# Performance work log

Hardware: AMD Instinct MI355X
Metric: run time of the kernel (lower is better)

Reference implementation:

```python
import jax, jax.numpy as jnp
import numpy as np

B, S, D, H = 4, 2048, 1024, 16
DH = D // H


def _rope_tables():
    # standard RoPE angle tables, shaped [1, S, 1, DH] as the module expects
    inv_freq = 1.0 / (10000.0 ** (np.arange(0, DH, 2, dtype=np.float32) / DH))
    ang = np.arange(S, dtype=np.float32)[:, None] * inv_freq[None, :]  # [S, DH/2]
    ang = np.concatenate([ang, ang], axis=-1)  # [S, DH]
    cos = jnp.asarray(np.cos(ang))[None, :, None, :]
    sin = jnp.asarray(np.sin(ang))[None, :, None, :]
    return cos, sin


def setup_inputs() -> dict:
    key = jax.random.key(0)
    ks = jax.random.split(key, 5)
    x = jax.random.normal(ks[0], (B, S, D), dtype=jnp.float32)
    wq = jax.random.normal(ks[1], (D, D), dtype=jnp.float32) * 0.02
    wk = jax.random.normal(ks[2], (D, D), dtype=jnp.float32) * 0.02
    wv = jax.random.normal(ks[3], (D, D), dtype=jnp.float32) * 0.02
    wo = jax.random.normal(ks[4], (D, D), dtype=jnp.float32) * 0.02
    cos, sin = _rope_tables()
    return {"x": x, "cos": cos, "sin": sin, "wq": wq, "wk": wk, "wv": wv, "wo": wo}


def _rotate_half(t):
    t1, t2 = t[..., : DH // 2], t[..., DH // 2:]
    return jnp.concatenate([-t2, t1], axis=-1)


def reference(x, cos, sin, wq, wk, wv, wo):
    b, s, d = x.shape
    # QKV projections (torch Linear: y = x @ W.T), reshape to [B, H, S, DH]
    q = (x @ wq.T).reshape(b, s, H, DH).transpose(0, 2, 1, 3)
    k = (x @ wk.T).reshape(b, s, H, DH).transpose(0, 2, 1, 3)
    v = (x @ wv.T).reshape(b, s, H, DH).transpose(0, 2, 1, 3)
    # permute(0,2,1,3): [1,S,1,DH] -> [1,1,S,DH]; slice [:, :s] is a no-op on the size-1 head dim
    cos_p = jnp.transpose(cos, (0, 2, 1, 3))[:, :s]
    sin_p = jnp.transpose(sin, (0, 2, 1, 3))[:, :s]
    q = q * cos_p + _rotate_half(q) * sin_p
    k = k * cos_p + _rotate_half(k) * sin_p
    # SDPA (no mask, dropout_p = 0)
    scores = jnp.einsum("bhqd,bhkd->bhqk", q, k) / jnp.sqrt(jnp.float32(DH))
    attn = jax.nn.softmax(scores, axis=-1)
    out = jnp.einsum("bhqk,bhkd->bhqd", attn, v)
    out = out.transpose(0, 2, 1, 3).reshape(b, s, d)
    return out @ wo.T
```

## Files before the change

kernel.cpp:

```cpp
#include <hip/hip_runtime.h>
#include <hip/hip_bf16.h>
#include <stdint.h>

#define B 4
#define S 2048
#define D 1024
#define H 16
#define DH 64
#define M_TOT (B*S)
#define BH (B*H)

typedef unsigned short u16;
typedef unsigned int u32;
typedef __attribute__((ext_vector_type(4))) float f32x4;
typedef __attribute__((ext_vector_type(16))) float f32x16;
typedef __attribute__((ext_vector_type(8))) short bf16x8;
typedef __attribute__((ext_vector_type(2))) unsigned int u32x2;

typedef const __attribute__((address_space(1))) unsigned int* gp_t;
typedef __attribute__((address_space(3))) unsigned int* lp_t;

__device__ __forceinline__ void gload_lds16(const void* g, void* l) {
    __builtin_amdgcn_global_load_lds((gp_t)g, (lp_t)l, 16, 0, 0);
}

__device__ __forceinline__ float bf2f(u16 u) {
    u32 t = ((u32)u) << 16;
    float f; __builtin_memcpy(&f, &t, 4); return f;
}
__device__ __forceinline__ u16 f2bf(float f) {
    u32 u; __builtin_memcpy(&u, &f, 4);
    u += 0x7fffu + ((u >> 16) & 1u);
    return (u16)(u >> 16);
}
__device__ __forceinline__ u32 packbf(float lo, float hi_) {
    __hip_bfloat162 h = __float22bfloat162_rn(float2{lo, hi_});
    u32 r; __builtin_memcpy(&r, &h, 4); return r;
}

__device__ __forceinline__ float exp2_fast(float x) { return __builtin_amdgcn_exp2f(x); }

#if __has_builtin(__builtin_amdgcn_permlane32_swap)
__device__ __forceinline__ void plswap(u32& a, u32& bb) {
    u32x2 r = __builtin_amdgcn_permlane32_swap(a, bb, false, false);
    a = r.x; bb = r.y;
}
#else
__device__ __forceinline__ void plswap(u32& a, u32& bb) {
    int hi = (threadIdx.x >> 5) & 1;
    u32 ra = (u32)__shfl_xor((int)a, 32);
    u32 rb = (u32)__shfl_xor((int)bb, 32);
    u32 na = hi ? rb : a;
    u32 nb = hi ? bb : ra;
    a = na; bb = nb;
}
#endif

__global__ __launch_bounds__(256)
void cvt_all_kernel(const float* __restrict__ x,
                    const float* __restrict__ wq, const float* __restrict__ wk,
                    const float* __restrict__ wv, const float* __restrict__ wo,
                    u16* __restrict__ xb, u16* __restrict__ wqb, u16* __restrict__ wkb,
                    u16* __restrict__ wvb, u16* __restrict__ wob)
{
    const size_t MD = (size_t)M_TOT * D;
    const size_t WD = (size_t)D * D;
    size_t i = ((size_t)blockIdx.x * 256 + threadIdx.x) * 8;
    const float* src; u16* dst; size_t off;
    if (i < MD) { src = x; dst = xb; off = i; }
    else {
        size_t j = i - MD;
        int wsel = (int)(j >> 20);
        off = j & (WD - 1);
        if      (wsel == 0) { src = wq; dst = wqb; }
        else if (wsel == 1) { src = wk; dst = wkb; }
        else if (wsel == 2) { src = wv; dst = wvb; }
        else                { src = wo; dst = wob; }
    }
    float4 a = *(const float4*)(src + off);
    float4 b = *(const float4*)(src + off + 4);
    union { u16 u[8]; bf16x8 v; } o;
    o.u[0] = f2bf(a.x); o.u[1] = f2bf(a.y); o.u[2] = f2bf(a.z); o.u[3] = f2bf(a.w);
    o.u[4] = f2bf(b.x); o.u[5] = f2bf(b.y); o.u[6] = f2bf(b.z); o.u[7] = f2bf(b.w);
    *(bf16x8*)(dst + off) = o.v;
}

template<int WRITE_BF16, int DO_ROPE>
__global__ __launch_bounds__(256)
void gemm_mfma(const u16* __restrict__ X,
               const u16* __restrict__ W0, const u16* __restrict__ W1, const u16* __restrict__ W2,
               void* Y0, void* Y1, void* Y2,
               const float* __restrict__ cosT, const float* __restrict__ sinT)
{
    __shared__ __align__(16) u16 Al[128 * 32];
    __shared__ __align__(16) u16 Bl[128 * 32];

    const u16* Wm = (blockIdx.z == 0) ? W0 : (blockIdx.z == 1) ? W1 : W2;
    void* Yv      = (blockIdx.z == 0) ? Y0 : (blockIdx.z == 1) ? Y1 : Y2;

    const int t = threadIdx.x;
    const int w = t >> 6, ll = t & 63;
    const int wr = w >> 1, wc = w & 1;
    const int g = ll >> 4, lc = ll & 15;
    const int m0 = blockIdx.x * 128, n0 = blockIdx.y * 128;

    const int srow = t >> 2;
    const int scol = (t & 3) * 8;

    const u16* Xa = X + (size_t)m0 * D;
    const u16* Wa = Wm + (size_t)n0 * D;

    f32x4 acc[4][4];
    #pragma unroll
    for (int i = 0; i < 4; ++i)
        #pragma unroll
        for (int j = 0; j < 4; ++j)
            acc[i][j] = (f32x4){0.f, 0.f, 0.f, 0.f};

    for (int k0 = 0; k0 < D; k0 += 32) {
        gload_lds16(Xa + (size_t)(srow)      * D + k0 + scol, &Al[(w * 64) * 8]);
        gload_lds16(Xa + (size_t)(64 + srow) * D + k0 + scol, &Al[(256 + w * 64) * 8]);
        gload_lds16(Wa + (size_t)(srow)      * D + k0 + scol, &Bl[(w * 64) * 8]);
        gload_lds16(Wa + (size_t)(64 + srow) * D + k0 + scol, &Bl[(256 + w * 64) * 8]);
        __syncthreads();

        bf16x8 af[4], bf[4];
        #pragma unroll
        for (int i = 0; i < 4; ++i)
            af[i] = *(const bf16x8*)&Al[(wr * 64 + i * 16 + lc) * 32 + g * 8];
        #pragma unroll
        for (int j = 0; j < 4; ++j)
            bf[j] = *(const bf16x8*)&Bl[(wc * 64 + j * 16 + lc) * 32 + g * 8];

        #pragma unroll
        for (int i = 0; i < 4; ++i)
            #pragma unroll
            for (int j = 0; j < 4; ++j)
                acc[i][j] = __builtin_amdgcn_mfma_f32_16x16x32_bf16(af[i], bf[j], acc[i][j], 0, 0, 0);
        __syncthreads();
    }

    if (DO_ROPE) {
        const float scale = (blockIdx.z == 0) ? (0.125f * 1.44269504f) : 1.0f;
        u16* Y = (u16*)Yv;
        #pragma unroll
        for (int i = 0; i < 4; ++i)
            #pragma unroll
            for (int r = 0; r < 4; ++r) {
                int row = m0 + wr * 64 + i * 16 + g * 4 + r;
                int s = row & (S - 1);
                #pragma unroll
                for (int jh = 0; jh < 2; ++jh) {
                    float c  = cosT[s * DH + jh * 16 + lc];
                    float sn = sinT[s * DH + jh * 16 + lc];
                    float a0 = acc[i][jh][r], a1 = acc[i][jh + 2][r];
                    size_t base = (size_t)row * D + n0 + wc * 64;
                    Y[base + jh * 16 + lc]       = f2bf((a0 * c - a1 * sn) * scale);
                    Y[base + (jh + 2) * 16 + lc] = f2bf((a1 * c + a0 * sn) * scale);
                }
            }
    } else if (WRITE_BF16) {
        u16* Y = (u16*)Yv;
        #pragma unroll
        for (int i = 0; i < 4; ++i)
            #pragma unroll
            for (int j = 0; j < 4; ++j)
                #pragma unroll
                for (int r = 0; r < 4; ++r) {
                    int row = m0 + wr * 64 + i * 16 + g * 4 + r;
                    int col = n0 + wc * 64 + j * 16 + lc;
                    Y[(size_t)row * D + col] = f2bf(acc[i][j][r]);
                }
    } else {
        float* Y = (float*)Yv;
        #pragma unroll
        for (int i = 0; i < 4; ++i)
            #pragma unroll
            for (int j = 0; j < 4; ++j)
                #pragma unroll
                for (int r = 0; r < 4; ++r) {
                    int row = m0 + wr * 64 + i * 16 + g * 4 + r;
                    int col = n0 + wc * 64 + j * 16 + lc;
                    Y[(size_t)row * D + col] = acc[i][j][r];
                }
    }
}

__global__ __launch_bounds__(256)
void vtrans_kernel(const u16* __restrict__ V, u16* __restrict__ Vt)
{
    __shared__ __align__(16) u16 Tl[64][72];
    const int t = threadIdx.x;
    const int s0 = blockIdx.x * 64;
    const int bh = blockIdx.y;
    const int b = bh >> 4, h = bh & 15;

    int sl = t >> 2, dh0 = (t & 3) * 16;
    const u16* src = &V[(size_t)(b * S + s0 + sl) * D + h * DH + dh0];
    bf16x8 v0 = *(const bf16x8*)src;
    bf16x8 v1 = *(const bf16x8*)(src + 8);
    #pragma unroll
    for (int i = 0; i < 8; ++i) {
        Tl[sl][dh0 + i]     = ((u16*)&v0)[i];
        Tl[sl][dh0 + 8 + i] = ((u16*)&v1)[i];
    }
    __syncthreads();
    int dh = t >> 2, ss0 = (t & 3) * 16;
    union { u16 u[16]; } o;
    #pragma unroll
    for (int i = 0; i < 16; ++i) o.u[i] = Tl[ss0 + i][dh];
    u16* dst = &Vt[((size_t)bh * DH + dh) * S + s0 + ss0];
    *(bf16x8*)dst       = *(bf16x8*)&o.u[0];
    *(bf16x8*)(dst + 8) = *(bf16x8*)&o.u[8];
}

#define QBLK 256
#define NT (S / 64)

__global__ __launch_bounds__(256, 2)
void attn_mfma(const u16* __restrict__ Q, const u16* __restrict__ Kg,
               const u16* __restrict__ Vt, u16* __restrict__ CTX)
{
    __shared__ __align__(16) u16 smem[16384];

    const int t  = threadIdx.x;
    const int w  = t >> 6;
    const int q  = t & 31;
    const int hi = (t >> 5) & 1;

    const int bid  = blockIdx.x;
    const int xcd  = bid & 7;
    const int slot = bid >> 3;
    const int bh   = xcd * 8 + (slot >> 3);
    const int qb   = slot & 7;
    const int b = bh >> 4, h = bh & 15;
    const int q0 = qb * QBLK;
    const int qbase = q0 + w * 64;

    bf16x8 qf[2][4];
    #pragma unroll
    for (int qg = 0; qg < 2; ++qg) {
        const u16* qp = &Q[(size_t)(b*S + qbase + qg*32 + q) * D + h*DH + hi*8];
        qf[qg][0] = *(const bf16x8*)(qp);
        qf[qg][1] = *(const bf16x8*)(qp + 16);
        qf[qg][2] = *(const bf16x8*)(qp + 32);
        qf[qg][3] = *(const bf16x8*)(qp + 48);
    }

    bf16x8 ones;
    {
        union { u16 u[8]; bf16x8 v; } ou;
        #pragma unroll
        for (int i = 0; i < 8; ++i) ou.u[i] = 0x3f80;
        ones = ou.v;
    }

    f32x16 po[4], lsum[2];
    #pragma unroll
    for (int i = 0; i < 16; ++i) {
        po[0][i] = 0.f; po[1][i] = 0.f; po[2][i] = 0.f; po[3][i] = 0.f;
        lsum[0][i] = 0.f; lsum[1][i] = 0.f;
    }

    const int srow = t >> 3;
    const int kbs  = ((t & 7) << 4) ^ ((srow & 7) << 4);
    const int scol = kbs >> 1;
    const int rsw  = (q & 7) << 4;

    u16* buf0 = smem;
    u16* buf1 = smem + 8192;

    const u16* kg = Kg + ((size_t)(b * S) + srow) * D + (size_t)h * DH + scol;
    const u16* vg = Vt + ((size_t)bh * DH + srow) * S + scol;
    const size_t KADV = (size_t)64 * D;

    #define STAGE(dst) do {                                   \
        gload_lds16(kg,           (dst) + w*512);             \
        gload_lds16(kg + 32*D,    (dst) + 2048 + w*512);      \
        gload_lds16(vg,           (dst) + 4096 + w*512);      \
        gload_lds16(vg + 32*S,    (dst) + 4096 + 2048 + w*512); \
        kg += KADV; vg += 64; } while (0)

    auto compute = [&](const u16* base) {
        const u16* Kl = base;
        const u16* Vl = base + 4096;
        f32x16 p00, p01, p10, p11;
        #pragma unroll
        for (int i = 0; i < 16; ++i) { p00[i]=0.f; p01[i]=0.f; p10[i]=0.f; p11[i]=0.f; }
        __builtin_amdgcn_s_setprio(1);
        #pragma unroll
        for (int c = 0; c < 4; ++c) {
            int cb = ((c*32 + hi*16) ^ rsw) >> 1;
            bf16x8 k0 = *(const bf16x8*)&Kl[(q << 6) + cb];
            bf16x8 k1 = *(const bf16x8*)&Kl[((32 + q) << 6) + cb];
            p00 = __builtin_amdgcn_mfma_f32_32x32x16_bf16(k0, qf[0][c], p00, 0, 0, 0);
            p01 = __builtin_amdgcn_mfma_f32_32x32x16_bf16(k1, qf[0][c], p01, 0, 0, 0);
            p10 = __builtin_amdgcn_mfma_f32_32x32x16_bf16(k0, qf[1][c], p10, 0, 0, 0);
            p11 = __builtin_amdgcn_mfma_f32_32x32x16_bf16(k1, qf[1][c], p11, 0, 0, 0);
        }
        __builtin_amdgcn_s_setprio(0);

        bf16x8 pa[2][4];
        #pragma unroll
        for (int qg = 0; qg < 2; ++qg) {
            const f32x16& e0 = qg ? p10 : p00;
            const f32x16& e1 = qg ? p11 : p01;
            u32 WW[16];
            #pragma unroll
            for (int j = 0; j < 8; ++j) {
                WW[j]     = packbf(exp2_fast(e0[2*j]), exp2_fast(e0[2*j + 1]));
                WW[8 + j] = packbf(exp2_fast(e1[2*j]), exp2_fast(e1[2*j + 1]));
            }
            #pragma unroll
            for (int ks = 0; ks < 4; ++ks) {
                const int b4 = 4*(ks & 1) + 8*(ks >> 1);
                u32 w0 = WW[b4 + 0], w1 = WW[b4 + 1], w2 = WW[b4 + 2], w3 = WW[b4 + 3];
                plswap(w0, w2);
                plswap(w1, w3);
                union { u32 u[4]; bf16x8 v; } pb;
                pb.u[0] = w0; pb.u[1] = w1; pb.u[2] = w2; pb.u[3] = w3;
                pa[qg][ks] = pb.v;
            }
        }

        __builtin_amdgcn_s_setprio(1);
        #pragma unroll
        for (int ks = 0; ks < 4; ++ks) {
            lsum[0] = __builtin_amdgcn_mfma_f32_32x32x16_bf16(ones, pa[0][ks], lsum[0], 0, 0, 0);
            lsum[1] = __builtin_amdgcn_mfma_f32_32x32x16_bf16(ones, pa[1][ks], lsum[1], 0, 0, 0);
        }
        #pragma unroll
        for (int ks = 0; ks < 4; ++ks) {
            int vb = ((ks*32 + hi*16) ^ rsw) >> 1;
            bf16x8 v0 = *(const bf16x8*)&Vl[(q << 6) + vb];
            bf16x8 v1 = *(const bf16x8*)&Vl[((32 + q) << 6) + vb];
            po[0] = __builtin_amdgcn_mfma_f32_32x32x16_bf16(v0, pa[0][ks], po[0], 0, 0, 0);
            po[1] = __builtin_amdgcn_mfma_f32_32x32x16_bf16(v1, pa[0][ks], po[1], 0, 0, 0);
            po[2] = __builtin_amdgcn_mfma_f32_32x32x16_bf16(v0, pa[1][ks], po[2], 0, 0, 0);
            po[3] = __builtin_amdgcn_mfma_f32_32x32x16_bf16(v1, pa[1][ks], po[3], 0, 0, 0);
        }
        __builtin_amdgcn_s_setprio(0);
    };

    STAGE(buf0);
    asm volatile("s_waitcnt vmcnt(0)" ::: "memory");
    __builtin_amdgcn_s_barrier();

    for (int ti = 0; ti < NT; ti += 2) {
        STAGE(buf1);
        compute(buf0);
        asm volatile("s_waitcnt vmcnt(0)" ::: "memory");
        __builtin_amdgcn_s_barrier();
        if (ti < NT - 2) STAGE(buf0);
        compute(buf1);
        asm volatile("s_waitcnt vmcnt(0)" ::: "memory");
        __builtin_amdgcn_s_barrier();
    }
    #undef STAGE

    u16* ow = &smem[w * 2304];
    #pragma unroll
    for (int qg = 0; qg < 2; ++qg) {
        float inv = 1.f / lsum[qg][0];
        #pragma unroll
        for (int r = 0; r < 16; ++r) {
            int d0 = (r & 3) + 8 * (r >> 2) + 4 * hi;
            ow[q * 72 + d0]      = f2bf(po[qg*2 + 0][r] * inv);
            ow[q * 72 + 32 + d0] = f2bf(po[qg*2 + 1][r] * inv);
        }
        int row = (t & 63) >> 1, half = t & 1;
        const u16* orow = &ow[row * 72 + half * 32];
        u16* gp = &CTX[(size_t)(b*S + qbase + qg*32 + row) * D + h*DH + half * 32];
        #pragma unroll
        for (int i = 0; i < 4; ++i)
            *(bf16x8*)(gp + i * 8) = *(const bf16x8*)(orow + i * 8);
    }
}

extern "C" void kernel_launch(void* const* d_in, const int* in_sizes, int n_in,
                              void* d_out, int out_size, void* d_ws, size_t ws_size,
                              hipStream_t stream)
{
    const float* x    = (const float*)d_in[0];
    const float* cosT = (const float*)d_in[1];
    const float* sinT = (const float*)d_in[2];
    const float* wq   = (const float*)d_in[3];
    const float* wk   = (const float*)d_in[4];
    const float* wv   = (const float*)d_in[5];
    const float* wo   = (const float*)d_in[6];
    float* out = (float*)d_out;

    const size_t MD = (size_t)M_TOT * D;
    const size_t WD = (size_t)D * D;

    u16* xb   = (u16*)d_ws;
    u16* Qb   = xb + MD;
    u16* Kb   = Qb + MD;
    u16* Vb   = Kb + MD;
    u16* Vtb  = Vb + MD;
    u16* CTXb = Vtb + MD;
    u16* wqb  = CTXb + MD;
    u16* wkb  = wqb + WD;
    u16* wvb  = wkb + WD;
    u16* wob  = wvb + WD;

    cvt_all_kernel<<<(int)((MD + 4*WD) / 8 / 256), 256, 0, stream>>>(
        x, wq, wk, wv, wo, xb, wqb, wkb, wvb, wob);

    gemm_mfma<1, 1><<<dim3(M_TOT / 128, D / 128, 2), 256, 0, stream>>>(
        xb, wqb, wkb, nullptr, Qb, Kb, nullptr, cosT, sinT);
    gemm_mfma<1, 0><<<dim3(M_TOT / 128, D / 128, 1), 256, 0, stream>>>(
        xb, wvb, nullptr, nullptr, Vb, nullptr, nullptr, nullptr, nullptr);

    vtrans_kernel<<<dim3(S / 64, BH), 256, 0, stream>>>(Vb, Vtb);

    attn_mfma<<<dim3(M_TOT / QBLK * H), 256, 0, stream>>>(Qb, Kb, Vtb, CTXb);

    gemm_mfma<0, 0><<<dim3(M_TOT / 128, D / 128, 1), 256, 0, stream>>>(
        CTXb, wob, nullptr, nullptr, out, nullptr, nullptr, nullptr, nullptr);
}
```

Baseline: 204.4 us.

## Merge V projection into QK GEMM launch and split attention compute into halves

The V projection now runs in the same GEMM launch as Q and K by adding a third grid z-slice, and RoPE is skipped when z is 2, which removes one kernel launch and tail. Inside the attention kernel the per-tile QK^T is computed in two key halves. Exp/pack and PV MFMAs for the first half are issued before the second half's packing, so VALU work can interleave with MFMA work. Accumulators now start from a zero vector instead of being zeroed each tile, and row-sum MFMAs are folded into the PV loops. The price is more register pressure and more reliance on the compiler to schedule the interleaving.

```diff
diff --git a/kernel.cpp b/kernel.cpp
--- a/kernel.cpp
+++ b/kernel.cpp
@@ -140,7 +140,7 @@
         __syncthreads();
     }
 
-    if (DO_ROPE) {
+    if (DO_ROPE && blockIdx.z < 2) {
         const float scale = (blockIdx.z == 0) ? (0.125f * 1.44269504f) : 1.0f;
         u16* Y = (u16*)Yv;
         #pragma unroll
@@ -255,11 +255,11 @@
         ones = ou.v;
     }
 
-    f32x16 po[4], lsum[2];
+    f32x16 po[4], lsum[2], zv;
     #pragma unroll
     for (int i = 0; i < 16; ++i) {
         po[0][i] = 0.f; po[1][i] = 0.f; po[2][i] = 0.f; po[3][i] = 0.f;
-        lsum[0][i] = 0.f; lsum[1][i] = 0.f;
+        lsum[0][i] = 0.f; lsum[1][i] = 0.f; zv[i] = 0.f;
     }
 
     const int srow = t >> 3;
@@ -281,63 +281,97 @@
         gload_lds16(vg + 32*S,    (dst) + 4096 + 2048 + w*512); \
         kg += KADV; vg += 64; } while (0)
 
+    #define PACK_HALF(pqg0, pqg1, pa00, pa01, pa10, pa11) do {            \
+        u32 W0[8], W1[8];                                                  \
+        _Pragma("unroll")                                                  \
+        for (int j = 0; j < 8; ++j) {                                      \
+            W0[j] = packbf(exp2_fast((pqg0)[2*j]), exp2_fast((pqg0)[2*j+1]));\
+            W1[j] = packbf(exp2_fast((pqg1)[2*j]), exp2_fast((pqg1)[2*j+1]));\
+        }                                                                  \
+        plswap(W0[0], W0[2]); plswap(W0[1], W0[3]);                        \
+        plswap(W0[4], W0[6]); plswap(W0[5], W0[7]);                        \
+        plswap(W1[0], W1[2]); plswap(W1[1], W1[3]);                        \
+        plswap(W1[4], W1[6]); plswap(W1[5], W1[7]);                        \
+        { union { u32 u[4]; bf16x8 v; } pb;                                \
+          pb.u[0]=W0[0]; pb.u[1]=W0[1]; pb.u[2]=W0[2]; pb.u[3]=W0[3]; (pa00)=pb.v; \
+          pb.u[0]=W0[4]; pb.u[1]=W0[5]; pb.u[2]=W0[6]; pb.u[3]=W0[7]; (pa01)=pb.v; \
+          pb.u[0]=W1[0]; pb.u[1]=W1[1]; pb.u[2]=W1[2]; pb.u[3]=W1[3]; (pa10)=pb.v; \
+          pb.u[0]=W1[4]; pb.u[1]=W1[5]; pb.u[2]=W1[6]; pb.u[3]=W1[7]; (pa11)=pb.v; } \
+    } while (0)
+
     auto compute = [&](const u16* base) {
         const u16* Kl = base;
         const u16* Vl = base + 4096;
-        f32x16 p00, p01, p10, p11;
-        #pragma unroll
-        for (int i = 0; i < 16; ++i) { p00[i]=0.f; p01[i]=0.f; p10[i]=0.f; p11[i]=0.f; }
+
+        f32x16 p00, p10, p01, p11;
+        {
+            bf16x8 k0[4];
+            #pragma unroll
+            for (int c = 0; c < 4; ++c)
+                k0[c] = *(const bf16x8*)&Kl[(q << 6) + ((( c*32 + hi*16) ^ rsw) >> 1)];
+            __builtin_amdgcn_s_setprio(1);
+            p00 = __builtin_amdgcn_mfma_f32_32x32x16_bf16(k0[0], qf[0][0], zv, 0, 0, 0);
+            p10 = __builtin_amdgcn_mfma_f32_32x32x16_bf16(k0[0], qf[1][0], zv, 0, 0, 0);
+            #pragma unroll
+            for (int c = 1; c < 4; ++c) {
+                p00 = __builtin_amdgcn_mfma_f32_32x32x16_bf16(k0[c], qf[0][c], p00, 0, 0, 0);
+                p10 = __builtin_amdgcn_mfma_f32_32x32x16_bf16(k0[c], qf[1][c], p10, 0, 0, 0);
+            }
+            __builtin_amdgcn_s_setprio(0);
+        }
+        {
+            bf16x8 k1[4];
+            #pragma unroll
+            for (int c = 0; c < 4; ++c)
+                k1[c] = *(const bf16x8*)&Kl[((32 + q) << 6) + (((c*32 + hi*16) ^ rsw) >> 1)];
+            __builtin_amdgcn_s_setprio(1);
+            p01 = __builtin_amdgcn_mfma_f32_32x32x16_bf16(k1[0], qf[0][0], zv, 0, 0, 0);
+            p11 = __builtin_amdgcn_mfma_f32_32x32x16_bf16(k1[0], qf[1][0], zv, 0, 0, 0);
+            #pragma unroll
+            for (int c = 1; c < 4; ++c) {
+                p01 = __builtin_amdgcn_mfma_f32_32x32x16_bf16(k1[c], qf[0][c], p01, 0, 0, 0);
+                p11 = __builtin_amdgcn_mfma_f32_32x32x16_bf16(k1[c], qf[1][c], p11, 0, 0, 0);
+            }
+            __builtin_amdgcn_s_setprio(0);
+        }
+
+        bf16x8 pa00, pa01, pa10, pa11;
+        PACK_HALF(p00, p10, pa00, pa01, pa10, pa11);
+
         __builtin_amdgcn_s_setprio(1);
         #pragma unroll
-        for (int c = 0; c < 4; ++c) {
-            int cb = ((c*32 + hi*16) ^ rsw) >> 1;
-            bf16x8 k0 = *(const bf16x8*)&Kl[(q << 6) + cb];
-            bf16x8 k1 = *(const bf16x8*)&Kl[((32 + q) << 6) + cb];
-            p00 = __builtin_amdgcn_mfma_f32_32x32x16_bf16(k0, qf[0][c], p00, 0, 0, 0);
-            p01 = __builtin_amdgcn_mfma_f32_32x32x16_bf16(k1, qf[0][c], p01, 0, 0, 0);
-            p10 = __builtin_amdgcn_mfma_f32_32x32x16_bf16(k0, qf[1][c], p10, 0, 0, 0);
-            p11 = __builtin_amdgcn_mfma_f32_32x32x16_bf16(k1, qf[1][c], p11, 0, 0, 0);
-        }
-        __builtin_amdgcn_s_setprio(0);
-
-        bf16x8 pa[2][4];
-        #pragma unroll
-        for (int qg = 0; qg < 2; ++qg) {
-            const f32x16& e0 = qg ? p10 : p00;
-            const f32x16& e1 = qg ? p11 : p01;
-            u32 WW[16];
-            #pragma unroll
-            for (int j = 0; j < 8; ++j) {
-                WW[j]     = packbf(exp2_fast(e0[2*j]), exp2_fast(e0[2*j + 1]));
-                WW[8 + j] = packbf(exp2_fast(e1[2*j]), exp2_fast(e1[2*j + 1]));
-            }
-            #pragma unroll
-            for (int ks = 0; ks < 4; ++ks) {
-                const int b4 = 4*(ks & 1) + 8*(ks >> 1);
-                u32 w0 = WW[b4 + 0], w1 = WW[b4 + 1], w2 = WW[b4 + 2], w3 = WW[b4 + 3];
-                plswap(w0, w2);
-                plswap(w1, w3);
-                union { u32 u[4]; bf16x8 v; } pb;
-                pb.u[0] = w0; pb.u[1] = w1; pb.u[2] = w2; pb.u[3] = w3;
-                pa[qg][ks] = pb.v;
-            }
-        }
-
-        __builtin_amdgcn_s_setprio(1);
-        #pragma unroll
-        for (int ks = 0; ks < 4; ++ks) {
-            lsum[0] = __builtin_amdgcn_mfma_f32_32x32x16_bf16(ones, pa[0][ks], lsum[0], 0, 0, 0);
-            lsum[1] = __builtin_amdgcn_mfma_f32_32x32x16_bf16(ones, pa[1][ks], lsum[1], 0, 0, 0);
-        }
-        #pragma unroll
-        for (int ks = 0; ks < 4; ++ks) {
+        for (int ks = 0; ks < 2; ++ks) {
             int vb = ((ks*32 + hi*16) ^ rsw) >> 1;
             bf16x8 v0 = *(const bf16x8*)&Vl[(q << 6) + vb];
             bf16x8 v1 = *(const bf16x8*)&Vl[((32 + q) << 6) + vb];
-            po[0] = __builtin_amdgcn_mfma_f32_32x32x16_bf16(v0, pa[0][ks], po[0], 0, 0, 0);
-            po[1] = __builtin_amdgcn_mfma_f32_32x32x16_bf16(v1, pa[0][ks], po[1], 0, 0, 0);
-            po[2] = __builtin_amdgcn_mfma_f32_32x32x16_bf16(v0, pa[1][ks], po[2], 0, 0, 0);
-            po[3] = __builtin_amdgcn_mfma_f32_32x32x16_bf16(v1, pa[1][ks], po[3], 0, 0, 0);
+            bf16x8 paq0 = ks ? pa01 : pa00;
+            bf16x8 paq1 = ks ? pa11 : pa10;
+            lsum[0] = __builtin_amdgcn_mfma_f32_32x32x16_bf16(ones, paq0, lsum[0], 0, 0, 0);
+            lsum[1] = __builtin_amdgcn_mfma_f32_32x32x16_bf16(ones, paq1, lsum[1], 0, 0, 0);
+            po[0] = __builtin_amdgcn_mfma_f32_32x32x16_bf16(v0, paq0, po[0], 0, 0, 0);
+            po[1] = __builtin_amdgcn_mfma_f32_32x32x16_bf16(v1, paq0, po[1], 0, 0, 0);
+            po[2] = __builtin_amdgcn_mfma_f32_32x32x16_bf16(v0, paq1, po[2], 0, 0, 0);
+            po[3] = __builtin_amdgcn_mfma_f32_32x32x16_bf16(v1, paq1, po[3], 0, 0, 0);
+        }
+        __builtin_amdgcn_s_setprio(0);
+
+        bf16x8 pb00, pb01, pb10, pb11;
+        PACK_HALF(p01, p11, pb00, pb01, pb10, pb11);
+
+        __builtin_amdgcn_s_setprio(1);
+        #pragma unroll
+        for (int ks = 0; ks < 2; ++ks) {
+            int vb = (((ks + 2)*32 + hi*16) ^ rsw) >> 1;
+            bf16x8 v0 = *(const bf16x8*)&Vl[(q << 6) + vb];
+            bf16x8 v1 = *(const bf16x8*)&Vl[((32 + q) << 6) + vb];
+            bf16x8 paq0 = ks ? pb01 : pb00;
+            bf16x8 paq1 = ks ? pb11 : pb10;
+            lsum[0] = __builtin_amdgcn_mfma_f32_32x32x16_bf16(ones, paq0, lsum[0], 0, 0, 0);
+            lsum[1] = __builtin_amdgcn_mfma_f32_32x32x16_bf16(ones, paq1, lsum[1], 0, 0, 0);
+            po[0] = __builtin_amdgcn_mfma_f32_32x32x16_bf16(v0, paq0, po[0], 0, 0, 0);
+            po[1] = __builtin_amdgcn_mfma_f32_32x32x16_bf16(v1, paq0, po[1], 0, 0, 0);
+            po[2] = __builtin_amdgcn_mfma_f32_32x32x16_bf16(v0, paq1, po[2], 0, 0, 0);
+            po[3] = __builtin_amdgcn_mfma_f32_32x32x16_bf16(v1, paq1, po[3], 0, 0, 0);
         }
         __builtin_amdgcn_s_setprio(0);
     };
@@ -357,6 +391,7 @@
         __builtin_amdgcn_s_barrier();
     }
     #undef STAGE
+    #undef PACK_HALF
 
     u16* ow = &smem[w * 2304];
     #pragma unroll
@@ -407,10 +442,8 @@
     cvt_all_kernel<<<(int)((MD + 4*WD) / 8 / 256), 256, 0, stream>>>(
         x, wq, wk, wv, wo, xb, wqb, wkb, wvb, wob);
 
-    gemm_mfma<1, 1><<<dim3(M_TOT / 128, D / 128, 2), 256, 0, stream>>>(
-        xb, wqb, wkb, nullptr, Qb, Kb, nullptr, cosT, sinT);
-    gemm_mfma<1, 0><<<dim3(M_TOT / 128, D / 128, 1), 256, 0, stream>>>(
-        xb, wvb, nullptr, nullptr, Vb, nullptr, nullptr, nullptr, nullptr);
+    gemm_mfma<1, 1><<<dim3(M_TOT / 128, D / 128, 3), 256, 0, stream>>>(
+        xb, wqb, wkb, wvb, Qb, Kb, Vb, cosT, sinT);
 
     vtrans_kernel<<<dim3(S / 64, BH), 256, 0, stream>>>(Vb, Vtb);
 
```

Result: no change. 202.5 us (-0.9%).

## Fuse V projection with transpose into QKV GEMM and widen attention KV tile

Applied to the files above, without the earlier changes.

The V projection now runs as a third z-slice of the fused QKV GEMM, and its epilogue writes the transposed V layout directly. This removes a separate GEMM launch, the standalone transpose kernel and the intermediate V buffer round trip. The attention kernel now stages 128-key tiles, which doubles shared memory per buffer, and computes scores per 32-key chunk using a new V swizzle. This shortens live register ranges and halves the barrier count, at the cost of more LDS per block and strided 8-byte scattered stores in the V epilogue.

```diff
diff --git a/kernel.cpp b/kernel.cpp
--- a/kernel.cpp
+++ b/kernel.cpp
@@ -140,7 +140,7 @@
         __syncthreads();
     }
 
-    if (DO_ROPE) {
+    if (DO_ROPE && blockIdx.z < 2) {
         const float scale = (blockIdx.z == 0) ? (0.125f * 1.44269504f) : 1.0f;
         u16* Y = (u16*)Yv;
         #pragma unroll
@@ -159,6 +159,21 @@
                     Y[base + (jh + 2) * 16 + lc] = f2bf((a1 * c + a0 * sn) * scale);
                 }
             }
+    } else if (DO_ROPE) {
+        u16* Y = (u16*)Yv;
+        #pragma unroll
+        for (int i = 0; i < 4; ++i)
+            #pragma unroll
+            for (int j = 0; j < 4; ++j) {
+                int row = m0 + wr * 64 + i * 16 + g * 4;
+                int col = n0 + wc * 64 + j * 16 + lc;
+                int bt = row >> 11, s = row & (S - 1);
+                size_t vtrow = (size_t)(bt * 16 + (col >> 6)) * 64 + (col & 63);
+                u32 w0 = packbf(acc[i][j][0], acc[i][j][1]);
+                u32 w1 = packbf(acc[i][j][2], acc[i][j][3]);
+                u32x2 pr; pr.x = w0; pr.y = w1;
+                *(u32x2*)&Y[vtrow * S + s] = pr;
+            }
     } else if (WRITE_BF16) {
         u16* Y = (u16*)Yv;
         #pragma unroll
@@ -186,42 +201,15 @@
     }
 }
 
-__global__ __launch_bounds__(256)
-void vtrans_kernel(const u16* __restrict__ V, u16* __restrict__ Vt)
-{
-    __shared__ __align__(16) u16 Tl[64][72];
-    const int t = threadIdx.x;
-    const int s0 = blockIdx.x * 64;
-    const int bh = blockIdx.y;
-    const int b = bh >> 4, h = bh & 15;
-
-    int sl = t >> 2, dh0 = (t & 3) * 16;
-    const u16* src = &V[(size_t)(b * S + s0 + sl) * D + h * DH + dh0];
-    bf16x8 v0 = *(const bf16x8*)src;
-    bf16x8 v1 = *(const bf16x8*)(src + 8);
-    #pragma unroll
-    for (int i = 0; i < 8; ++i) {
-        Tl[sl][dh0 + i]     = ((u16*)&v0)[i];
-        Tl[sl][dh0 + 8 + i] = ((u16*)&v1)[i];
-    }
-    __syncthreads();
-    int dh = t >> 2, ss0 = (t & 3) * 16;
-    union { u16 u[16]; } o;
-    #pragma unroll
-    for (int i = 0; i < 16; ++i) o.u[i] = Tl[ss0 + i][dh];
-    u16* dst = &Vt[((size_t)bh * DH + dh) * S + s0 + ss0];
-    *(bf16x8*)dst       = *(bf16x8*)&o.u[0];
-    *(bf16x8*)(dst + 8) = *(bf16x8*)&o.u[8];
-}
-
 #define QBLK 256
-#define NT (S / 64)
+#define KVT 128
+#define NT (S / KVT)
 
 __global__ __launch_bounds__(256, 2)
 void attn_mfma(const u16* __restrict__ Q, const u16* __restrict__ Kg,
                const u16* __restrict__ Vt, u16* __restrict__ CTX)
 {
-    __shared__ __align__(16) u16 smem[16384];
+    __shared__ __align__(16) u16 smem[32768];
 
     const int t  = threadIdx.x;
     const int w  = t >> 6;
@@ -255,91 +243,96 @@
         ones = ou.v;
     }
 
-    f32x16 po[4], lsum[2];
+    f32x16 po[4], lsum[2], zv;
     #pragma unroll
     for (int i = 0; i < 16; ++i) {
         po[0][i] = 0.f; po[1][i] = 0.f; po[2][i] = 0.f; po[3][i] = 0.f;
-        lsum[0][i] = 0.f; lsum[1][i] = 0.f;
-    }
-
-    const int srow = t >> 3;
-    const int kbs  = ((t & 7) << 4) ^ ((srow & 7) << 4);
-    const int scol = kbs >> 1;
+        lsum[0][i] = 0.f; lsum[1][i] = 0.f; zv[i] = 0.f;
+    }
+
+    const int ksrow = t >> 3;
+    const int kscol = (((t & 7) << 4) ^ ((ksrow & 7) << 4)) >> 1;
+    const int vsrow = t >> 4;
+    const int vscol = (((t & 15) ^ (vsrow & 15)) << 3);
     const int rsw  = (q & 7) << 4;
+    const int vsw  = (q & 15) << 4;
 
     u16* buf0 = smem;
-    u16* buf1 = smem + 8192;
-
-    const u16* kg = Kg + ((size_t)(b * S) + srow) * D + (size_t)h * DH + scol;
-    const u16* vg = Vt + ((size_t)bh * DH + srow) * S + scol;
-    const size_t KADV = (size_t)64 * D;
-
-    #define STAGE(dst) do {                                   \
-        gload_lds16(kg,           (dst) + w*512);             \
-        gload_lds16(kg + 32*D,    (dst) + 2048 + w*512);      \
-        gload_lds16(vg,           (dst) + 4096 + w*512);      \
-        gload_lds16(vg + 32*S,    (dst) + 4096 + 2048 + w*512); \
-        kg += KADV; vg += 64; } while (0)
+    u16* buf1 = smem + 16384;
+
+    const u16* kg = Kg + ((size_t)(b * S) + ksrow) * D + (size_t)h * DH + kscol;
+    const u16* vg = Vt + ((size_t)bh * DH + vsrow) * S + vscol;
+
+    #define STAGE(dst) do {                                         \
+        gload_lds16(kg,           (dst) + 0*2048 + w*512);          \
+        gload_lds16(kg + 32*D,    (dst) + 1*2048 + w*512);          \
+        gload_lds16(kg + 64*D,    (dst) + 2*2048 + w*512);          \
+        gload_lds16(kg + 96*D,    (dst) + 3*2048 + w*512);          \
+        gload_lds16(vg,           (dst) + 8192 + 0*2048 + w*512);   \
+        gload_lds16(vg + 16*S,    (dst) + 8192 + 1*2048 + w*512);   \
+        gload_lds16(vg + 32*S,    (dst) + 8192 + 2*2048 + w*512);   \
+        gload_lds16(vg + 48*S,    (dst) + 8192 + 3*2048 + w*512);   \
+        kg += (size_t)KVT * D; vg += KVT; } while (0)
 
     auto compute = [&](const u16* base) {
         const u16* Kl = base;
-        const u16* Vl = base + 4096;
-        f32x16 p00, p01, p10, p11;
-        #pragma unroll
-        for (int i = 0; i < 16; ++i) { p00[i]=0.f; p01[i]=0.f; p10[i]=0.f; p11[i]=0.f; }
-        __builtin_amdgcn_s_setprio(1);
+        const u16* Vl = base + 8192;
         #pragma unroll
         for (int c = 0; c < 4; ++c) {
-            int cb = ((c*32 + hi*16) ^ rsw) >> 1;
-            bf16x8 k0 = *(const bf16x8*)&Kl[(q << 6) + cb];
-            bf16x8 k1 = *(const bf16x8*)&Kl[((32 + q) << 6) + cb];
-            p00 = __builtin_amdgcn_mfma_f32_32x32x16_bf16(k0, qf[0][c], p00, 0, 0, 0);
-            p01 = __builtin_amdgcn_mfma_f32_32x32x16_bf16(k1, qf[0][c], p01, 0, 0, 0);
-            p10 = __builtin_amdgcn_mfma_f32_32x32x16_bf16(k0, qf[1][c], p10, 0, 0, 0);
-            p11 = __builtin_amdgcn_mfma_f32_32x32x16_bf16(k1, qf[1][c], p11, 0, 0, 0);
+            f32x16 p0, p1;
+            {
+                const u16* kr = &Kl[(c*32 + q) << 6];
+                bf16x8 k0 = *(const bf16x8*)&kr[((0*32 + hi*16) ^ rsw) >> 1];
+                __builtin_amdgcn_s_setprio(1);
+                p0 = __builtin_amdgcn_mfma_f32_32x32x16_bf16(k0, qf[0][0], zv, 0, 0, 0);
+                p1 = __builtin_amdgcn_mfma_f32_32x32x16_bf16(k0, qf[1][0], zv, 0, 0, 0);
+                #pragma unroll
+                for (int cc = 1; cc < 4; ++cc) {
+                    bf16x8 kf = *(const bf16x8*)&kr[((cc*32 + hi*16) ^ rsw) >> 1];
+                    p0 = __builtin_amdgcn_mfma_f32_32x32x16_bf16(kf, qf[0][cc], p0, 0, 0, 0);
+                    p1 = __builtin_amdgcn_mfma_f32_32x32x16_bf16(kf, qf[1][cc], p1, 0, 0, 0);
+                }
+                __builtin_amdgcn_s_setprio(0);
+            }
+
+            u32 W0[8], W1[8];
+            #pragma unroll
+            for (int j = 0; j < 8; ++j) {
+                W0[j] = packbf(exp2_fast(p0[2*j]), exp2_fast(p0[2*j + 1]));
+                W1[j] = packbf(exp2_fast(p1[2*j]), exp2_fast(p1[2*j + 1]));
+            }
+            plswap(W0[0], W0[2]); plswap(W0[1], W0[3]);
+            plswap(W0[4], W0[6]); plswap(W0[5], W0[7]);
+            plswap(W1[0], W1[2]); plswap(W1[1], W1[3]);
+            plswap(W1[4], W1[6]); plswap(W1[5], W1[7]);
+            bf16x8 pa0a, pa0b, pa1a, pa1b;
+            {
+                union { u32 u[4]; bf16x8 v; } pb;
+                pb.u[0]=W0[0]; pb.u[1]=W0[1]; pb.u[2]=W0[2]; pb.u[3]=W0[3]; pa0a = pb.v;
+                pb.u[0]=W0[4]; pb.u[1]=W0[5]; pb.u[2]=W0[6]; pb.u[3]=W0[7]; pa0b = pb.v;
+                pb.u[0]=W1[0]; pb.u[1]=W1[1]; pb.u[2]=W1[2]; pb.u[3]=W1[3]; pa1a = pb.v;
+                pb.u[0]=W1[4]; pb.u[1]=W1[5]; pb.u[2]=W1[6]; pb.u[3]=W1[7]; pa1b = pb.v;
+            }
+
+            __builtin_amdgcn_s_setprio(1);
+            lsum[0] = __builtin_amdgcn_mfma_f32_32x32x16_bf16(ones, pa0a, lsum[0], 0, 0, 0);
+            lsum[1] = __builtin_amdgcn_mfma_f32_32x32x16_bf16(ones, pa1a, lsum[1], 0, 0, 0);
+            lsum[0] = __builtin_amdgcn_mfma_f32_32x32x16_bf16(ones, pa0b, lsum[0], 0, 0, 0);
+            lsum[1] = __builtin_amdgcn_mfma_f32_32x32x16_bf16(ones, pa1b, lsum[1], 0, 0, 0);
+            #pragma unroll
+            for (int kk = 0; kk < 2; ++kk) {
+                int vb = ((c*64 + kk*32 + hi*16) ^ vsw) >> 1;
+                bf16x8 v0 = *(const bf16x8*)&Vl[(q << 7) + vb];
+                bf16x8 v1 = *(const bf16x8*)&Vl[((32 + q) << 7) + vb];
+                bf16x8 pq0 = kk ? pa0b : pa0a;
+                bf16x8 pq1 = kk ? pa1b : pa1a;
+                po[0] = __builtin_amdgcn_mfma_f32_32x32x16_bf16(v0, pq0, po[0], 0, 0, 0);
+                po[1] = __builtin_amdgcn_mfma_f32_32x32x16_bf16(v1, pq0, po[1], 0, 0, 0);
+                po[2] = __builtin_amdgcn_mfma_f32_32x32x16_bf16(v0, pq1, po[2], 0, 0, 0);
+                po[3] = __builtin_amdgcn_mfma_f32_32x32x16_bf16(v1, pq1, po[3], 0, 0, 0);
+            }
+            __builtin_amdgcn_s_setprio(0);
         }
-        __builtin_amdgcn_s_setprio(0);
-
-        bf16x8 pa[2][4];
-        #pragma unroll
-        for (int qg = 0; qg < 2; ++qg) {
-            const f32x16& e0 = qg ? p10 : p00;
-            const f32x16& e1 = qg ? p11 : p01;
-            u32 WW[16];
-            #pragma unroll
-            for (int j = 0; j < 8; ++j) {
-                WW[j]     = packbf(exp2_fast(e0[2*j]), exp2_fast(e0[2*j + 1]));
-                WW[8 + j] = packbf(exp2_fast(e1[2*j]), exp2_fast(e1[2*j + 1]));
-            }
-            #pragma unroll
-            for (int ks = 0; ks < 4; ++ks) {
-                const int b4 = 4*(ks & 1) + 8*(ks >> 1);
-                u32 w0 = WW[b4 + 0], w1 = WW[b4 + 1], w2 = WW[b4 + 2], w3 = WW[b4 + 3];
-                plswap(w0, w2);
-                plswap(w1, w3);
-                union { u32 u[4]; bf16x8 v; } pb;
-                pb.u[0] = w0; pb.u[1] = w1; pb.u[2] = w2; pb.u[3] = w3;
-                pa[qg][ks] = pb.v;
-            }
-        }
-
-        __builtin_amdgcn_s_setprio(1);
-        #pragma unroll
-        for (int ks = 0; ks < 4; ++ks) {
-            lsum[0] = __builtin_amdgcn_mfma_f32_32x32x16_bf16(ones, pa[0][ks], lsum[0], 0, 0, 0);
-            lsum[1] = __builtin_amdgcn_mfma_f32_32x32x16_bf16(ones, pa[1][ks], lsum[1], 0, 0, 0);
-        }
-        #pragma unroll
-        for (int ks = 0; ks < 4; ++ks) {
-            int vb = ((ks*32 + hi*16) ^ rsw) >> 1;
-            bf16x8 v0 = *(const bf16x8*)&Vl[(q << 6) + vb];
-            bf16x8 v1 = *(const bf16x8*)&Vl[((32 + q) << 6) + vb];
-            po[0] = __builtin_amdgcn_mfma_f32_32x32x16_bf16(v0, pa[0][ks], po[0], 0, 0, 0);
-            po[1] = __builtin_amdgcn_mfma_f32_32x32x16_bf16(v1, pa[0][ks], po[1], 0, 0, 0);
-            po[2] = __builtin_amdgcn_mfma_f32_32x32x16_bf16(v0, pa[1][ks], po[2], 0, 0, 0);
-            po[3] = __builtin_amdgcn_mfma_f32_32x32x16_bf16(v1, pa[1][ks], po[3], 0, 0, 0);
-        }
-        __builtin_amdgcn_s_setprio(0);
     };
 
     STAGE(buf0);
@@ -396,8 +389,7 @@
     u16* xb   = (u16*)d_ws;
     u16* Qb   = xb + MD;
     u16* Kb   = Qb + MD;
-    u16* Vb   = Kb + MD;
-    u16* Vtb  = Vb + MD;
+    u16* Vtb  = Kb + MD;
     u16* CTXb = Vtb + MD;
     u16* wqb  = CTXb + MD;
     u16* wkb  = wqb + WD;
@@ -407,12 +399,8 @@
     cvt_all_kernel<<<(int)((MD + 4*WD) / 8 / 256), 256, 0, stream>>>(
         x, wq, wk, wv, wo, xb, wqb, wkb, wvb, wob);
 
-    gemm_mfma<1, 1><<<dim3(M_TOT / 128, D / 128, 2), 256, 0, stream>>>(
-        xb, wqb, wkb, nullptr, Qb, Kb, nullptr, cosT, sinT);
-    gemm_mfma<1, 0><<<dim3(M_TOT / 128, D / 128, 1), 256, 0, stream>>>(
-        xb, wvb, nullptr, nullptr, Vb, nullptr, nullptr, nullptr, nullptr);
-
-    vtrans_kernel<<<dim3(S / 64, BH), 256, 0, stream>>>(Vb, Vtb);
+    gemm_mfma<1, 1><<<dim3(M_TOT / 128, D / 128, 3), 256, 0, stream>>>(
+        xb, wqb, wkb, wvb, Qb, Kb, Vtb, cosT, sinT);
 
     attn_mfma<<<dim3(M_TOT / QBLK * H), 256, 0, stream>>>(Qb, Kb, Vtb, CTXb);
 
```

Result: faster. 185.6 us (median of 2 runs) (-9.2%).
